# Kernel tuning notes

Hardware: AMD Instinct MI355X
Metric: run time of the kernel (lower is better)

The kernel has to match this reference:

```python
import jax, jax.numpy as jnp
import numpy as np

EPS = 1e-5

def _layer_norm(x, gamma, beta):
    mu = jnp.mean(x, axis=-1, keepdims=True)
    var = jnp.mean(jnp.square(x - mu), axis=-1, keepdims=True)
    return (x - mu) * jax.lax.rsqrt(var + EPS) * gamma + beta

def setup_inputs() -> dict:
    key = jax.random.key(0)
    ks = jax.random.split(key, 6)
    B, D, H = 8192, 1024, 1024
    x = jax.random.normal(ks[0], (B, D), dtype=jnp.float32)
    h0 = jax.random.normal(ks[1], (B, H), dtype=jnp.float32)
    c0 = jax.random.normal(ks[2], (B, H), dtype=jnp.float32)
    # learned params (orthogonal init approximated by scaled normal for reference purposes)
    weight_h = jax.random.normal(ks[3], (H, 4 * H), dtype=jnp.float32) / np.sqrt(H)
    weight_x = jax.random.normal(ks[4], (D, 4 * H), dtype=jnp.float32) / np.sqrt(D)
    bias = jnp.zeros((4 * H,), dtype=jnp.float32).at[:H].set(1.0)  # forget-gate bias init to 1
    ln1_g = jnp.ones((4 * H,), jnp.float32); ln1_b = jnp.zeros((4 * H,), jnp.float32)
    ln2_g = jnp.ones((4 * H,), jnp.float32); ln2_b = jnp.zeros((4 * H,), jnp.float32)
    ln3_g = jnp.ones((H,), jnp.float32); ln3_b = jnp.zeros((H,), jnp.float32)
    return {"x": x, "h0": h0, "c0": c0, "weight_h": weight_h, "weight_x": weight_x,
            "bias": bias, "ln1_g": ln1_g, "ln1_b": ln1_b, "ln2_g": ln2_g, "ln2_b": ln2_b,
            "ln3_g": ln3_g, "ln3_b": ln3_b}

def reference(x, h0, c0, weight_h, weight_x, bias, ln1_g, ln1_b, ln2_g, ln2_b, ln3_g, ln3_b):
    # gates: [B, 4H] = LN(h0 @ Wh) + LN(x @ Wx) + bias
    gates = _layer_norm(h0 @ weight_h, ln1_g, ln1_b) + _layer_norm(x @ weight_x, ln2_g, ln2_b) + bias
    H = h0.shape[-1]
    f_g, i_g, o_g, c_g = jnp.split(gates, 4, axis=1)  # forget, in, out, cell
    c1 = jax.nn.sigmoid(f_g) * c0 + jax.nn.sigmoid(i_g) * jnp.tanh(c_g)
    h1 = jax.nn.sigmoid(o_g) * jnp.tanh(_layer_norm(c1, ln3_g, ln3_b))
    return (h1, c1)
```

## Files before the change

### kernel.cpp

```cpp
#include <hip/hip_runtime.h>
#include <cstdint>

#define B_ROWS 8192
#define KDIM 1024
#define N4 4096

typedef __attribute__((ext_vector_type(8))) short short8;
typedef __attribute__((ext_vector_type(4))) float float4v;

__device__ __forceinline__ unsigned short f2bf(float f) {
  union { float f; unsigned int u; } v; v.f = f;
  unsigned int r = v.u + 0x7fffu + ((v.u >> 16) & 1u);
  return (unsigned short)(r >> 16);
}

__device__ __forceinline__ float bf2f(unsigned short s) {
  union { unsigned int u; float f; } v; v.u = ((unsigned int)s) << 16;
  return v.f;
}

__device__ __forceinline__ void async16(const unsigned short* g, unsigned short* l) {
  auto gp = (const __attribute__((address_space(1))) unsigned int*)(uintptr_t)g;
  auto lp = (__attribute__((address_space(3))) unsigned int*)(unsigned int)(uintptr_t)l;
  __builtin_amdgcn_global_load_lds(gp, lp, 16, 0, 0);
}

__device__ __forceinline__ float sigm(float v) { return 1.f / (1.f + expf(-v)); }


__global__ __launch_bounds__(256) void cast_bf16(const float* __restrict__ in0,
                                                 unsigned short* __restrict__ out0,
                                                 const float* __restrict__ in1,
                                                 unsigned short* __restrict__ out1) {
  const float* in = blockIdx.y ? in1 : in0;
  unsigned short* out = blockIdx.y ? out1 : out0;
  int i = (blockIdx.x * 256 + threadIdx.x) * 4;
  float4 v = *(const float4*)(in + i);
  ushort4 o;
  o.x = f2bf(v.x); o.y = f2bf(v.y); o.z = f2bf(v.z); o.w = f2bf(v.w);
  *(ushort4*)(out + i) = o;
}

__global__ __launch_bounds__(256) void pack_b(const float* __restrict__ W0,
                                              unsigned short* __restrict__ P0,
                                              const float* __restrict__ W1,
                                              unsigned short* __restrict__ P1) {
  const float* W = blockIdx.z ? W1 : W0;
  unsigned short* P = blockIdx.z ? P1 : P0;
  const int ti = blockIdx.x;
  const int c  = blockIdx.y * 4 + (threadIdx.x >> 6);
  const int l  = threadIdx.x & 63;
  const int n  = ti * 16 + (l & 15);
  const int k0 = c * 32 + (l >> 4) * 8;
  unsigned short o[8];
#pragma unroll
  for (int j = 0; j < 8; ++j)
    o[j] = f2bf(W[(size_t)(k0 + j) * N4 + n]);
  *(short8*)(P + ((size_t)(ti * 32 + c) * 64 + l) * 8) = *(short8*)o;
}


__global__ __launch_bounds__(256) void gemm_bf16(
    const unsigned short* __restrict__ Ah, const unsigned short* __restrict__ Bph,
    unsigned short* __restrict__ Uh,
    const unsigned short* __restrict__ Ax, const unsigned short* __restrict__ Bpx,
    unsigned short* __restrict__ Ux, int row0) {
  const unsigned short* A; const unsigned short* Bp; unsigned short* U;
  if (blockIdx.z == 0) { A = Ah; Bp = Bph; U = Uh; } else { A = Ax; Bp = Bpx; U = Ux; }

  __shared__ unsigned short ldsA[2][128 * 64];

  const int tid = threadIdx.x;
  const int wave = tid >> 6;
  const int lane = tid & 63;
  const int wm = (wave & 1) * 64;
  const int wn = (wave >> 1) * 64;

  const int m0 = row0 + blockIdx.y * 128;
  const int n0 = blockIdx.x * 128;

  const int r8 = lane >> 3;
  const int c8 = lane & 7;
  const int g8 = (c8 - r8) & 7;
  const unsigned short* gA0 = A + (size_t)(m0 + wave * 32 + r8) * KDIM + g8 * 8;
  const int lA0 = (wave * 32) * 64;

  const unsigned short* bBase = Bp + (size_t)((n0 + wn) >> 4) * 16384 + (size_t)lane * 8;

  float4v acc[4][4];
  float4v zero = {0.f, 0.f, 0.f, 0.f};
#pragma unroll
  for (int i = 0; i < 4; ++i)
#pragma unroll
    for (int j = 0; j < 4; ++j) acc[i][j] = zero;

  short8 b0[2][4], b1[2][4];

#define DMA_A(kt, buf)                                                         \
  {                                                                            \
    _Pragma("unroll")                                                          \
    for (int j = 0; j < 4; ++j)                                                \
      async16(gA0 + (kt) * 64 + j * 8 * KDIM, &ldsA[buf][lA0 + j * 8 * 64]);   \
  }

#define LOAD_B(kt, breg)                                                       \
  {                                                                            \
    _Pragma("unroll")                                                          \
    for (int kh = 0; kh < 2; ++kh) {                                           \
      const int c = (kt) * 2 + kh;                                             \
      _Pragma("unroll")                                                        \
      for (int i = 0; i < 4; ++i)                                              \
        breg[kh][i] = *(const short8*)(bBase + i * 16384 + c * 512);           \
    }                                                                          \
  }

#define COMPUTE(buf, breg)                                                     \
  {                                                                            \
    _Pragma("unroll")                                                          \
    for (int kh = 0; kh < 2; ++kh) {                                           \
      short8 a[4];                                                             \
      _Pragma("unroll")                                                        \
      for (int i = 0; i < 4; ++i) {                                            \
        const int ma = wm + i * 16 + (lane & 15);                              \
        const int q = kh * 4 + (lane >> 4);                                    \
        a[i] = *(const short8*)(&ldsA[buf][ma * 64 + ((q + ma) & 7) * 8]);     \
      }                                                                        \
      _Pragma("unroll")                                                        \
      for (int mi = 0; mi < 4; ++mi)                                           \
        _Pragma("unroll")                                                      \
        for (int ni = 0; ni < 4; ++ni)                                         \
          acc[mi][ni] = __builtin_amdgcn_mfma_f32_16x16x32_bf16(               \
              a[mi], breg[kh][ni], acc[mi][ni], 0, 0, 0);                      \
    }                                                                          \
  }

  DMA_A(0, 0);
  LOAD_B(0, b0);

  for (int p = 0; p < 8; ++p) {
    const int t0 = 2 * p;
    __syncthreads();
    DMA_A(t0 + 1, 1);
    LOAD_B(t0 + 1, b1);
    COMPUTE(0, b0);
    __syncthreads();
    if (p != 7) {
      DMA_A(t0 + 2, 0);
      LOAD_B(t0 + 2, b0);
    }
    COMPUTE(1, b1);
  }

  const int colc = lane & 15;
  const int rowq = (lane >> 4) * 4;
  unsigned short* Ub = U + (size_t)(blockIdx.y * 128 + wm + rowq) * N4 + n0 + wn + colc;
#pragma unroll
  for (int mi = 0; mi < 4; ++mi)
#pragma unroll
    for (int r = 0; r < 4; ++r) {
      unsigned short* Urow = Ub + (size_t)(mi * 16 + r) * N4;
#pragma unroll
      for (int ni = 0; ni < 4; ++ni) Urow[ni * 16] = f2bf(acc[mi][ni][r]);
    }
#undef DMA_A
#undef LOAD_B
#undef COMPUTE
}


__global__ __launch_bounds__(256) void fused_ln_lstm(
    const unsigned short* __restrict__ Uh, const unsigned short* __restrict__ Ux,
    const float* __restrict__ c0, const float* __restrict__ bias,
    const float* __restrict__ g1, const float* __restrict__ b1,
    const float* __restrict__ g2, const float* __restrict__ b2,
    const float* __restrict__ g3, const float* __restrict__ b3,
    float* __restrict__ h1o, float* __restrict__ c1o, int row0) {
  const int t = threadIdx.x;
  const int lane = t & 63;
  const int wv = t >> 6;
  const size_t rloc = blockIdx.x;
  const size_t rabs = rloc + (size_t)row0;

  const ushort4* uh = (const ushort4*)(Uh + rloc * N4);
  const ushort4* ux = (const ushort4*)(Ux + rloc * N4);
  float4 cold = ((const float4*)(c0 + rabs * KDIM))[t];

  float4 vh[4], vx[4];
  float sh = 0.f, qh = 0.f, sx = 0.f, qx = 0.f;
#pragma unroll
  for (int k = 0; k < 4; ++k) {
    ushort4 au = uh[k * 256 + t];
    float4 a; a.x = bf2f(au.x); a.y = bf2f(au.y); a.z = bf2f(au.z); a.w = bf2f(au.w);
    vh[k] = a;
    sh += (a.x + a.y) + (a.z + a.w);
    qh += a.x * a.x + a.y * a.y + a.z * a.z + a.w * a.w;
    ushort4 bu = ux[k * 256 + t];
    float4 b; b.x = bf2f(bu.x); b.y = bf2f(bu.y); b.z = bf2f(bu.z); b.w = bf2f(bu.w);
    vx[k] = b;
    sx += (b.x + b.y) + (b.z + b.w);
    qx += b.x * b.x + b.y * b.y + b.z * b.z + b.w * b.w;
  }
  __shared__ float red[4][4];
#pragma unroll
  for (int o = 32; o > 0; o >>= 1) {
    sh += __shfl_down(sh, o); qh += __shfl_down(qh, o);
    sx += __shfl_down(sx, o); qx += __shfl_down(qx, o);
  }
  if (lane == 0) { red[wv][0] = sh; red[wv][1] = qh; red[wv][2] = sx; red[wv][3] = qx; }
  __syncthreads();
  sh = red[0][0] + red[1][0] + red[2][0] + red[3][0];
  qh = red[0][1] + red[1][1] + red[2][1] + red[3][1];
  sx = red[0][2] + red[1][2] + red[2][2] + red[3][2];
  qx = red[0][3] + red[1][3] + red[2][3] + red[3][3];
  const float inv4 = 1.f / 4096.f;
  const float muh = sh * inv4, mux = sx * inv4;
  const float rsh = rsqrtf(qh * inv4 - muh * muh + 1e-5f);
  const float rsx = rsqrtf(qx * inv4 - mux * mux + 1e-5f);

  float4 gate[4];
#pragma unroll
  for (int k = 0; k < 4; ++k) {
    int j = k * 256 + t;
    float4 G1 = ((const float4*)g1)[j], B1 = ((const float4*)b1)[j];
    float4 G2 = ((const float4*)g2)[j], B2 = ((const float4*)b2)[j];
    float4 BB = ((const float4*)bias)[j];
    float4 a = vh[k], b = vx[k], r;
    r.x = (a.x - muh) * rsh * G1.x + B1.x + (b.x - mux) * rsx * G2.x + B2.x + BB.x;
    r.y = (a.y - muh) * rsh * G1.y + B1.y + (b.y - mux) * rsx * G2.y + B2.y + BB.y;
    r.z = (a.z - muh) * rsh * G1.z + B1.z + (b.z - mux) * rsx * G2.z + B2.z + BB.z;
    r.w = (a.w - muh) * rsh * G1.w + B1.w + (b.w - mux) * rsx * G2.w + B2.w + BB.w;
    gate[k] = r;
  }
  float4 fg = gate[0], ig = gate[1], og = gate[2], cg = gate[3];
  float4 c1v;
  c1v.x = sigm(fg.x) * cold.x + sigm(ig.x) * tanhf(cg.x);
  c1v.y = sigm(fg.y) * cold.y + sigm(ig.y) * tanhf(cg.y);
  c1v.z = sigm(fg.z) * cold.z + sigm(ig.z) * tanhf(cg.z);
  c1v.w = sigm(fg.w) * cold.w + sigm(ig.w) * tanhf(cg.w);

  float sc = (c1v.x + c1v.y) + (c1v.z + c1v.w);
  float qc = c1v.x * c1v.x + c1v.y * c1v.y + c1v.z * c1v.z + c1v.w * c1v.w;
#pragma unroll
  for (int o = 32; o > 0; o >>= 1) { sc += __shfl_down(sc, o); qc += __shfl_down(qc, o); }
  __syncthreads();
  if (lane == 0) { red[wv][0] = sc; red[wv][1] = qc; }
  __syncthreads();
  sc = red[0][0] + red[1][0] + red[2][0] + red[3][0];
  qc = red[0][1] + red[1][1] + red[2][1] + red[3][1];
  const float invH = 1.f / 1024.f;
  const float muc = sc * invH;
  const float rsc = rsqrtf(qc * invH - muc * muc + 1e-5f);
  float4 G3 = ((const float4*)g3)[t], B3 = ((const float4*)b3)[t];
  float4 h1v;
  h1v.x = sigm(og.x) * tanhf((c1v.x - muc) * rsc * G3.x + B3.x);
  h1v.y = sigm(og.y) * tanhf((c1v.y - muc) * rsc * G3.y + B3.y);
  h1v.z = sigm(og.z) * tanhf((c1v.z - muc) * rsc * G3.z + B3.z);
  h1v.w = sigm(og.w) * tanhf((c1v.w - muc) * rsc * G3.w + B3.w);

  ((float4*)(h1o + rabs * KDIM))[t] = h1v;
  ((float4*)(c1o + rabs * KDIM))[t] = c1v;
}


extern "C" void kernel_launch(void* const* d_in, const int* in_sizes, int n_in,
                              void* d_out, int out_size, void* d_ws, size_t ws_size,
                              hipStream_t stream) {
  const float* x    = (const float*)d_in[0];
  const float* h0   = (const float*)d_in[1];
  const float* c0   = (const float*)d_in[2];
  const float* Wh   = (const float*)d_in[3];
  const float* Wx   = (const float*)d_in[4];
  const float* bias = (const float*)d_in[5];
  const float* g1   = (const float*)d_in[6];
  const float* b1   = (const float*)d_in[7];
  const float* g2   = (const float*)d_in[8];
  const float* b2   = (const float*)d_in[9];
  const float* g3   = (const float*)d_in[10];
  const float* b3   = (const float*)d_in[11];
  float* h1o = (float*)d_out;
  float* c1o = h1o + (size_t)B_ROWS * KDIM;

  unsigned short* Ah  = (unsigned short*)d_ws;
  unsigned short* Ax  = Ah + (size_t)B_ROWS * KDIM;
  unsigned short* Bph = Ax + (size_t)B_ROWS * KDIM;
  unsigned short* Bpx = Bph + (size_t)N4 * KDIM;
  unsigned short* U = Bpx + (size_t)N4 * KDIM;
  size_t used = ((size_t)B_ROWS * KDIM * 2 + (size_t)N4 * KDIM * 2) * sizeof(unsigned short);
  size_t rem = ws_size > used ? ws_size - used : 0;
  int chunk = (int)(rem / ((size_t)2 * N4 * sizeof(unsigned short)));
  chunk &= ~127;
  if (chunk > B_ROWS) chunk = B_ROWS;
  if (chunk < 128) chunk = 128;

  cast_bf16<<<dim3(B_ROWS * KDIM / 1024, 2), 256, 0, stream>>>(h0, Ah, x, Ax);
  pack_b<<<dim3(N4 / 16, 8, 2), 256, 0, stream>>>(Wh, Bph, Wx, Bpx);

  for (int r0 = 0; r0 < B_ROWS; r0 += chunk) {
    int rows = chunk;
    if (r0 + rows > B_ROWS) rows = B_ROWS - r0;
    unsigned short* Uh = U;
    unsigned short* Ux = U + (size_t)rows * N4;
    gemm_bf16<<<dim3(N4 / 128, rows / 128, 2), 256, 0, stream>>>(Ah, Bph, Uh, Ax, Bpx, Ux, r0);
    fused_ln_lstm<<<rows, 256, 0, stream>>>(Uh, Ux, c0, bias, g1, b1, g2, b2, g3, b3, h1o, c1o, r0);
  }
}
```

Baseline: 389.5 us.

## Pre-pack A into MFMA fragment layout and load both operands directly from global

Replaces the plain bf16 cast of h0/x with a pack kernel that lays A out in the same per-lane MFMA fragment order as B. The GEMM then drops the LDS staging, async global-to-LDS copies and barriers, and instead loads A and B fragments straight into registers with a two-stage register double buffer. Launch bounds now request 3 blocks per CU. Each wave now re-reads its A tiles from global/L2 rather than sharing them through LDS, which raises cache traffic in exchange for removing LDS and sync overhead.

New measurement: 470.3 us. 1.21x slower.

```diff
diff --git a/kernel.cpp b/kernel.cpp
--- a/kernel.cpp
+++ b/kernel.cpp
@@ -19,26 +19,26 @@
   return v.f;
 }
 
-__device__ __forceinline__ void async16(const unsigned short* g, unsigned short* l) {
-  auto gp = (const __attribute__((address_space(1))) unsigned int*)(uintptr_t)g;
-  auto lp = (__attribute__((address_space(3))) unsigned int*)(unsigned int)(uintptr_t)l;
-  __builtin_amdgcn_global_load_lds(gp, lp, 16, 0, 0);
-}
-
 __device__ __forceinline__ float sigm(float v) { return 1.f / (1.f + expf(-v)); }
 
 
-__global__ __launch_bounds__(256) void cast_bf16(const float* __restrict__ in0,
-                                                 unsigned short* __restrict__ out0,
-                                                 const float* __restrict__ in1,
-                                                 unsigned short* __restrict__ out1) {
-  const float* in = blockIdx.y ? in1 : in0;
-  unsigned short* out = blockIdx.y ? out1 : out0;
-  int i = (blockIdx.x * 256 + threadIdx.x) * 4;
-  float4 v = *(const float4*)(in + i);
-  ushort4 o;
-  o.x = f2bf(v.x); o.y = f2bf(v.y); o.z = f2bf(v.z); o.w = f2bf(v.w);
-  *(ushort4*)(out + i) = o;
+__global__ __launch_bounds__(256) void pack_a(const float* __restrict__ in0,
+                                              unsigned short* __restrict__ out0,
+                                              const float* __restrict__ in1,
+                                              unsigned short* __restrict__ out1) {
+  const float* A = blockIdx.z ? in1 : in0;
+  unsigned short* P = blockIdx.z ? out1 : out0;
+  const int ti = blockIdx.x;
+  const int kc = blockIdx.y * 4 + (threadIdx.x >> 6);
+  const int l  = threadIdx.x & 63;
+  const int row = ti * 16 + (l & 15);
+  const int k0  = kc * 32 + (l >> 4) * 8;
+  const float4 v0 = *(const float4*)(A + (size_t)row * KDIM + k0);
+  const float4 v1 = *(const float4*)(A + (size_t)row * KDIM + k0 + 4);
+  unsigned short o[8];
+  o[0] = f2bf(v0.x); o[1] = f2bf(v0.y); o[2] = f2bf(v0.z); o[3] = f2bf(v0.w);
+  o[4] = f2bf(v1.x); o[5] = f2bf(v1.y); o[6] = f2bf(v1.z); o[7] = f2bf(v1.w);
+  *(short8*)(P + ((size_t)(ti * 32 + kc) * 64 + l) * 8) = *(short8*)o;
 }
 
 __global__ __launch_bounds__(256) void pack_b(const float* __restrict__ W0,
@@ -60,32 +60,24 @@
 }
 
 
-__global__ __launch_bounds__(256) void gemm_bf16(
-    const unsigned short* __restrict__ Ah, const unsigned short* __restrict__ Bph,
+__global__ __launch_bounds__(256, 3) void gemm_bf16(
+    const unsigned short* __restrict__ Aph, const unsigned short* __restrict__ Bph,
     unsigned short* __restrict__ Uh,
-    const unsigned short* __restrict__ Ax, const unsigned short* __restrict__ Bpx,
+    const unsigned short* __restrict__ Apx, const unsigned short* __restrict__ Bpx,
     unsigned short* __restrict__ Ux, int row0) {
-  const unsigned short* A; const unsigned short* Bp; unsigned short* U;
-  if (blockIdx.z == 0) { A = Ah; Bp = Bph; U = Uh; } else { A = Ax; Bp = Bpx; U = Ux; }
-
-  __shared__ unsigned short ldsA[2][128 * 64];
-
-  const int tid = threadIdx.x;
-  const int wave = tid >> 6;
-  const int lane = tid & 63;
+  const unsigned short* Ap; const unsigned short* Bp; unsigned short* U;
+  if (blockIdx.z == 0) { Ap = Aph; Bp = Bph; U = Uh; } else { Ap = Apx; Bp = Bpx; U = Ux; }
+
+  const int wave = threadIdx.x >> 6;
+  const int lane = threadIdx.x & 63;
   const int wm = (wave & 1) * 64;
   const int wn = (wave >> 1) * 64;
 
   const int m0 = row0 + blockIdx.y * 128;
   const int n0 = blockIdx.x * 128;
 
-  const int r8 = lane >> 3;
-  const int c8 = lane & 7;
-  const int g8 = (c8 - r8) & 7;
-  const unsigned short* gA0 = A + (size_t)(m0 + wave * 32 + r8) * KDIM + g8 * 8;
-  const int lA0 = (wave * 32) * 64;
-
-  const unsigned short* bBase = Bp + (size_t)((n0 + wn) >> 4) * 16384 + (size_t)lane * 8;
+  const short8* aB = (const short8*)Ap + (size_t)((m0 + wm) >> 4) * 2048 + lane;
+  const short8* bB = (const short8*)Bp + (size_t)((n0 + wn) >> 4) * 2048 + lane;
 
   float4v acc[4][4];
   float4v zero = {0.f, 0.f, 0.f, 0.f};
@@ -94,62 +86,37 @@
 #pragma unroll
     for (int j = 0; j < 4; ++j) acc[i][j] = zero;
 
-  short8 b0[2][4], b1[2][4];
-
-#define DMA_A(kt, buf)                                                         \
+  short8 aC[4], bC[4], aN[4], bN[4];
+
+#define LOADF(kc, ar, br)                                                      \
   {                                                                            \
     _Pragma("unroll")                                                          \
-    for (int j = 0; j < 4; ++j)                                                \
-      async16(gA0 + (kt) * 64 + j * 8 * KDIM, &ldsA[buf][lA0 + j * 8 * 64]);   \
-  }
-
-#define LOAD_B(kt, breg)                                                       \
+    for (int i = 0; i < 4; ++i) {                                              \
+      ar[i] = aB[(size_t)i * 2048 + (kc) * 64];                                \
+      br[i] = bB[(size_t)i * 2048 + (kc) * 64];                                \
+    }                                                                          \
+  }
+
+#define MFMA16(ar, br)                                                         \
   {                                                                            \
     _Pragma("unroll")                                                          \
-    for (int kh = 0; kh < 2; ++kh) {                                           \
-      const int c = (kt) * 2 + kh;                                             \
+    for (int mi = 0; mi < 4; ++mi)                                             \
       _Pragma("unroll")                                                        \
-      for (int i = 0; i < 4; ++i)                                              \
-        breg[kh][i] = *(const short8*)(bBase + i * 16384 + c * 512);           \
-    }                                                                          \
-  }
-
-#define COMPUTE(buf, breg)                                                     \
-  {                                                                            \
-    _Pragma("unroll")                                                          \
-    for (int kh = 0; kh < 2; ++kh) {                                           \
-      short8 a[4];                                                             \
-      _Pragma("unroll")                                                        \
-      for (int i = 0; i < 4; ++i) {                                            \
-        const int ma = wm + i * 16 + (lane & 15);                              \
-        const int q = kh * 4 + (lane >> 4);                                    \
-        a[i] = *(const short8*)(&ldsA[buf][ma * 64 + ((q + ma) & 7) * 8]);     \
-      }                                                                        \
-      _Pragma("unroll")                                                        \
-      for (int mi = 0; mi < 4; ++mi)                                           \
-        _Pragma("unroll")                                                      \
-        for (int ni = 0; ni < 4; ++ni)                                         \
-          acc[mi][ni] = __builtin_amdgcn_mfma_f32_16x16x32_bf16(               \
-              a[mi], breg[kh][ni], acc[mi][ni], 0, 0, 0);                      \
-    }                                                                          \
-  }
-
-  DMA_A(0, 0);
-  LOAD_B(0, b0);
-
-  for (int p = 0; p < 8; ++p) {
-    const int t0 = 2 * p;
-    __syncthreads();
-    DMA_A(t0 + 1, 1);
-    LOAD_B(t0 + 1, b1);
-    COMPUTE(0, b0);
-    __syncthreads();
-    if (p != 7) {
-      DMA_A(t0 + 2, 0);
-      LOAD_B(t0 + 2, b0);
-    }
-    COMPUTE(1, b1);
-  }
+      for (int ni = 0; ni < 4; ++ni)                                           \
+        acc[mi][ni] = __builtin_amdgcn_mfma_f32_16x16x32_bf16(                 \
+            ar[mi], br[ni], acc[mi][ni], 0, 0, 0);                             \
+  }
+
+  LOADF(0, aC, bC);
+#pragma unroll
+  for (int kc = 0; kc < 32; kc += 2) {
+    LOADF(kc + 1, aN, bN);
+    MFMA16(aC, bC);
+    if (kc + 2 < 32) LOADF(kc + 2, aC, bC);
+    MFMA16(aN, bN);
+  }
+#undef LOADF
+#undef MFMA16
 
   const int colc = lane & 15;
   const int rowq = (lane >> 4) * 4;
@@ -162,9 +129,6 @@
 #pragma unroll
       for (int ni = 0; ni < 4; ++ni) Urow[ni * 16] = f2bf(acc[mi][ni][r]);
     }
-#undef DMA_A
-#undef LOAD_B
-#undef COMPUTE
 }
 
 
@@ -280,9 +244,9 @@
   float* h1o = (float*)d_out;
   float* c1o = h1o + (size_t)B_ROWS * KDIM;
 
-  unsigned short* Ah  = (unsigned short*)d_ws;
-  unsigned short* Ax  = Ah + (size_t)B_ROWS * KDIM;
-  unsigned short* Bph = Ax + (size_t)B_ROWS * KDIM;
+  unsigned short* Aph = (unsigned short*)d_ws;
+  unsigned short* Apx = Aph + (size_t)B_ROWS * KDIM;
+  unsigned short* Bph = Apx + (size_t)B_ROWS * KDIM;
   unsigned short* Bpx = Bph + (size_t)N4 * KDIM;
   unsigned short* U = Bpx + (size_t)N4 * KDIM;
   size_t used = ((size_t)B_ROWS * KDIM * 2 + (size_t)N4 * KDIM * 2) * sizeof(unsigned short);
@@ -292,7 +256,7 @@
   if (chunk > B_ROWS) chunk = B_ROWS;
   if (chunk < 128) chunk = 128;
 
-  cast_bf16<<<dim3(B_ROWS * KDIM / 1024, 2), 256, 0, stream>>>(h0, Ah, x, Ax);
+  pack_a<<<dim3(B_ROWS / 16, 8, 2), 256, 0, stream>>>(h0, Aph, x, Apx);
   pack_b<<<dim3(N4 / 16, 8, 2), 256, 0, stream>>>(Wh, Bph, Wx, Bpx);
 
   for (int r0 = 0; r0 < B_ROWS; r0 += chunk) {
@@ -300,7 +264,7 @@
     if (r0 + rows > B_ROWS) rows = B_ROWS - r0;
     unsigned short* Uh = U;
     unsigned short* Ux = U + (size_t)rows * N4;
-    gemm_bf16<<<dim3(N4 / 128, rows / 128, 2), 256, 0, stream>>>(Ah, Bph, Uh, Ax, Bpx, Ux, r0);
+    gemm_bf16<<<dim3(N4 / 128, rows / 128, 2), 256, 0, stream>>>(Aph, Bph, Uh, Apx, Bpx, Ux, r0);
     fused_ln_lstm<<<rows, 256, 0, stream>>>(Uh, Ux, c0, bias, g1, b1, g2, b2, g3, b3, h1o, c1o, r0);
   }
 }
```
